# Performance work log

Hardware: AMD Instinct MI355X
Metric: run time of the kernel (lower is better)

The kernel has to match this reference:

```python
import jax, jax.numpy as jnp
import numpy as np

B, S, H, F, E, N, K = 2, 4096, 1024, 3584, 8, 2, 2


def setup_inputs() -> dict:
    key = jax.random.key(0)
    ks = jax.random.split(key, 6)
    scale_h = 1.0 / np.sqrt(H)
    scale_f = 1.0 / np.sqrt(F)
    return {
        "hidden_states": jax.random.normal(ks[0], (B, S, H), dtype=jnp.float32),
        "gate_w": jax.random.normal(ks[1], (E, H), dtype=jnp.float32) * scale_h,
        "gate2_w": jax.random.normal(ks[2], (N, H), dtype=jnp.float32) * scale_h,
        "w1": jax.random.normal(ks[3], (E, F, H), dtype=jnp.float32) * scale_h,
        "w2": jax.random.normal(ks[4], (E, H, F), dtype=jnp.float32) * scale_f,
        "w3": jax.random.normal(ks[5], (E, F, H), dtype=jnp.float32) * scale_h,
    }


def reference(hidden_states, gate_w, gate2_w, w1, w2, w3):
    b, s, h = hidden_states.shape
    x = hidden_states.reshape(-1, h)  # [T, H]

    # Router: real gate + null-expert gate, concatenated
    router_logits = jnp.concatenate([x @ gate_w.T, x @ gate2_w.T], axis=1)  # [T, E+N]
    rw = jax.nn.softmax(router_logits.astype(jnp.float32), axis=1)
    top_w, sel = jax.lax.top_k(rw, K)  # [T, K]

    # Null experts (idx >= E) get their raw weight; real experts are renormalized
    mask = sel < E
    sw = top_w * mask
    denom = sw.sum(axis=-1, keepdims=True)
    denom = jnp.where(denom == 0, 1.0, denom)
    weights = (sw / denom + top_w * (~mask)).astype(x.dtype)  # [T, K]

    # Per-(token, real-expert) combine weight; null experts drop out (one_hot -> 0)
    combine = jnp.einsum("tke,tk->et", jax.nn.one_hot(sel, E, dtype=x.dtype), weights)  # [E, T]

    def body(acc, p):
        w1e, w2e, w3e, cw = p
        hgate = jax.nn.silu(x @ w1e.T) * (x @ w3e.T)  # [T, F]
        return acc + cw[:, None] * (hgate @ w2e.T), None

    out, _ = jax.lax.scan(body, jnp.zeros_like(x), (w1, w2, w3, combine))
    return out.reshape(b, s, h), router_logits
```

## Files before the change

kernel.cpp:

```cpp
#include <hip/hip_runtime.h>
#include <hip/hip_bf16.h>

namespace {

constexpr int T_TOK = 8192;
constexpr int HDIM  = 1024;
constexpr int FDIM  = 3584;
constexpr int CAP_ROWS = 17408;
constexpr int MAXMT = CAP_ROWS / 128;

typedef __bf16 bf16x8 __attribute__((ext_vector_type(8)));
typedef float  f32x4  __attribute__((ext_vector_type(4)));

#define CFENCE() asm volatile("" ::: "memory")

__device__ inline unsigned short f2bf(float f) {
  union { float f; unsigned u; } a; a.f = f;
  unsigned r = a.u + 0x7fffu + ((a.u >> 16) & 1u);
  return (unsigned short)(r >> 16);
}

typedef const __attribute__((address_space(1))) void* gptr_t;
typedef __attribute__((address_space(3))) void* lptr_t;
__device__ inline void gload_lds16(const void* g, void* l) {
  __builtin_amdgcn_global_load_lds((gptr_t)g, (lptr_t)l, 16, 0, 0);
}

__global__ __launch_bounds__(256) void k_router(
    const float* __restrict__ x, const float* __restrict__ gw,
    const float* __restrict__ gw2, float* __restrict__ logits_out,
    int* __restrict__ sel, float* __restrict__ wts)
{
  int t = blockIdx.x * 4 + (threadIdx.x >> 6);
  int lane = threadIdx.x & 63;
  if (t >= T_TOK) return;
  const float* xr = x + (size_t)t * HDIM;
  float acc[10];
#pragma unroll
  for (int e = 0; e < 10; ++e) acc[e] = 0.f;
#pragma unroll
  for (int it = 0; it < 4; ++it) {
    int base = it * 256 + lane * 4;
    float4 xv = *reinterpret_cast<const float4*>(xr + base);
#pragma unroll
    for (int e = 0; e < 8; ++e) {
      float4 g = *reinterpret_cast<const float4*>(gw + e * HDIM + base);
      acc[e] += xv.x * g.x + xv.y * g.y + xv.z * g.z + xv.w * g.w;
    }
#pragma unroll
    for (int e = 0; e < 2; ++e) {
      float4 g = *reinterpret_cast<const float4*>(gw2 + e * HDIM + base);
      acc[8 + e] += xv.x * g.x + xv.y * g.y + xv.z * g.z + xv.w * g.w;
    }
  }
#pragma unroll
  for (int e = 0; e < 10; ++e) {
#pragma unroll
    for (int off = 32; off > 0; off >>= 1)
      acc[e] += __shfl_xor(acc[e], off, 64);
  }
  if (lane == 0) {
    float* lo = logits_out + (size_t)t * 10;
#pragma unroll
    for (int e = 0; e < 10; ++e) lo[e] = acc[e];
    float mx = acc[0];
#pragma unroll
    for (int e = 1; e < 10; ++e) mx = fmaxf(mx, acc[e]);
    float p[10], s = 0.f;
#pragma unroll
    for (int e = 0; e < 10; ++e) { p[e] = __expf(acc[e] - mx); s += p[e]; }
    float inv = 1.f / s;
#pragma unroll
    for (int e = 0; e < 10; ++e) p[e] *= inv;
    int i0 = 0;
    for (int e = 1; e < 10; ++e) if (p[e] > p[i0]) i0 = e;
    int i1 = (i0 == 0) ? 1 : 0;
    for (int e = 0; e < 10; ++e) if (e != i0 && p[e] > p[i1]) i1 = e;
    float w0 = p[i0], w1 = p[i1];
    bool r0 = i0 < 8, r1 = i1 < 8;
    float den = (r0 ? w0 : 0.f) + (r1 ? w1 : 0.f);
    if (den == 0.f) den = 1.f;
    sel[t * 2]     = i0; wts[t * 2]     = r0 ? w0 / den : 0.f;
    sel[t * 2 + 1] = i1; wts[t * 2 + 1] = r1 ? w1 / den : 0.f;
  }
}

__global__ __launch_bounds__(256) void k_histseg(
    const int* __restrict__ sel, int* __restrict__ meta)
{
  __shared__ int part[256][8];
  __shared__ int s_tile0[9];
  int tid = threadIdx.x;
  int c[8];
#pragma unroll
  for (int e = 0; e < 8; ++e) c[e] = 0;
  for (int i = 0; i < 64; ++i) {
    int v = sel[i * 256 + tid];
#pragma unroll
    for (int e = 0; e < 8; ++e) c[e] += (v == e);
  }
#pragma unroll
  for (int e = 0; e < 8; ++e) part[tid][e] = c[e];
  __syncthreads();
  for (int s = 128; s >= 1; s >>= 1) {
    if (tid < s) {
#pragma unroll
      for (int e = 0; e < 8; ++e) part[tid][e] += part[tid + s][e];
    }
    __syncthreads();
  }
  if (tid == 0) {
    int off = 0;
    for (int e = 0; e < 8; ++e) {
      int cnt = part[0][e];
      meta[e] = cnt;
      meta[8 + e] = 0;
      meta[16 + e] = off;
      s_tile0[e] = off >> 7;
      off += (cnt + 127) & ~127;
    }
    meta[24] = off;
    meta[25] = off >> 7;
    s_tile0[8] = off >> 7;
  }
  __syncthreads();
  int nt = s_tile0[8];
  if (tid < nt) {
    int e = 0;
    while (s_tile0[e + 1] <= tid) ++e;
    meta[32 + tid] = e;
  }
}

__global__ __launch_bounds__(256) void k_zeropad(
    const int* __restrict__ meta, unsigned short* __restrict__ xg)
{
  int e = blockIdx.x >> 7, r = blockIdx.x & 127;
  int c = meta[e];
  int pad = (c + 127) & ~127;
  if (c + r >= pad) return;
  size_t row = (size_t)meta[16 + e] + c + r;
  reinterpret_cast<ushort4*>(xg + row * HDIM)[threadIdx.x] = ushort4{0, 0, 0, 0};
}

__global__ __launch_bounds__(256) void k_scatter(
    const float* __restrict__ x, const int* __restrict__ sel,
    int* __restrict__ meta, int* __restrict__ pair_row,
    unsigned short* __restrict__ xg)
{
  __shared__ int s_cnt[8];
  __shared__ int s_base[8];
  __shared__ int s_row[256];
  int tid = threadIdx.x;
  int pair0 = blockIdx.x * 256;
  if (tid < 8) s_cnt[tid] = 0;
  __syncthreads();
  int e = sel[pair0 + tid];
  int rank = -1;
  if (e < 8) rank = atomicAdd(&s_cnt[e], 1);
  __syncthreads();
  if (tid < 8) {
    int c = s_cnt[tid];
    s_base[tid] = c > 0 ? atomicAdd(&meta[8 + tid], c) : 0;
  }
  __syncthreads();
  int row = (e < 8) ? meta[16 + e] + s_base[e] + rank : -1;
  pair_row[pair0 + tid] = row;
  s_row[tid] = row;
  __syncthreads();
  int wid = tid >> 6, lane = tid & 63;
  for (int i = wid; i < 256; i += 4) {
    int r = s_row[i];
    if (r < 0) continue;
    const float* xr = x + (size_t)((pair0 + i) >> 1) * HDIM;
    unsigned short* dst = xg + (size_t)r * HDIM;
#pragma unroll
    for (int it = 0; it < 4; ++it) {
      int base = it * 256 + lane * 4;
      float4 v = *reinterpret_cast<const float4*>(xr + base);
      ushort4 o{f2bf(v.x), f2bf(v.y), f2bf(v.z), f2bf(v.w)};
      *reinterpret_cast<ushort4*>(dst + base) = o;
    }
  }
}

__global__ __launch_bounds__(256) void k_conv3(
    const float* __restrict__ s1, const float* __restrict__ s3,
    const float* __restrict__ s2,
    unsigned short* __restrict__ d1, unsigned short* __restrict__ d3,
    unsigned short* __restrict__ d2,
    long long total, long long rl13, long long ss13,
    long long rl2, long long ss2)
{
  long long i = ((long long)blockIdx.x * 256 + threadIdx.x) * 8;
  if (i >= total) return;
  const float* src; unsigned short* dst; long long rowlen, sstride;
  if (blockIdx.y == 0)      { src = s1; dst = d1; rowlen = rl13; sstride = ss13; }
  else if (blockIdx.y == 1) { src = s3; dst = d3; rowlen = rl13; sstride = ss13; }
  else                      { src = s2; dst = d2; rowlen = rl2;  sstride = ss2;  }
  const float* sp;
  if (rowlen == sstride) {
    sp = src + i;
  } else {
    long long r = i / rowlen, c = i - r * rowlen;
    sp = src + r * sstride + c;
  }
  float4 a = reinterpret_cast<const float4*>(sp)[0];
  float4 b = reinterpret_cast<const float4*>(sp)[1];
  ushort4* d = reinterpret_cast<ushort4*>(dst + i);
  d[0] = ushort4{f2bf(a.x), f2bf(a.y), f2bf(a.z), f2bf(a.w)};
  d[1] = ushort4{f2bf(b.x), f2bf(b.y), f2bf(b.z), f2bf(b.w)};
}

__global__ __launch_bounds__(256) void k_gemm1(
    const unsigned short* __restrict__ xg,
    const unsigned short* __restrict__ wc1,
    const unsigned short* __restrict__ wc3,
    unsigned short* __restrict__ hg,
    const int* __restrict__ meta, int Fc)
{
  __shared__ __attribute__((aligned(128))) char lds[65536];

  int mt = blockIdx.y;
  if (mt >= meta[25]) return;
  int e = meta[32 + mt];
  int mrow0 = mt * 128;
  int fl0 = blockIdx.x * 64;

  int tid = threadIdx.x, wid = tid >> 6, lane = tid & 63;
  int lr = lane & 15, lg = lane >> 4;
  int wm = wid >> 1, wn = wid & 1;

  f32x4 acc1[4][2], acc3[4][2];
  const f32x4 zero = {0.f, 0.f, 0.f, 0.f};
#pragma unroll
  for (int m = 0; m < 4; ++m)
#pragma unroll
    for (int n = 0; n < 2; ++n) { acc1[m][n] = zero; acc3[m][n] = zero; }

  const unsigned short* w1p = wc1 + ((size_t)e * Fc + fl0) * HDIM;
  const unsigned short* w3p = wc3 + ((size_t)e * Fc + fl0) * HDIM;

  int srow = tid >> 3;
  int c8 = (tid & 7) ^ (srow & 7);

  const unsigned short* pa[4];
  const unsigned short* pb1[2];
  const unsigned short* pb3[2];
#pragma unroll
  for (int i = 0; i < 4; ++i)
    pa[i] = xg + (size_t)(mrow0 + i * 32 + srow) * HDIM + c8 * 8;
#pragma unroll
  for (int i = 0; i < 2; ++i) {
    pb1[i] = w1p + (size_t)(i * 32 + srow) * HDIM + c8 * 8;
    pb3[i] = w3p + (size_t)(i * 32 + srow) * HDIM + c8 * 8;
  }

  auto STAGE = [&](int buf) {
    char* base = lds + buf * 32768;
#pragma unroll
    for (int i = 0; i < 4; ++i) {
      gload_lds16(pa[i], base + i * 4096 + wid * 1024);
      pa[i] += 64;
    }
#pragma unroll
    for (int i = 0; i < 2; ++i) {
      gload_lds16(pb1[i], base + 16384 + i * 4096 + wid * 1024);
      pb1[i] += 64;
      gload_lds16(pb3[i], base + 24576 + i * 4096 + wid * 1024);
      pb3[i] += 64;
    }
  };

  auto COMPUTE = [&](int buf) {
    const char* base = lds + buf * 32768;
#pragma unroll
    for (int kk = 0; kk < 2; ++kk) {
      bf16x8 a[4], b1[2], b3[2];
#pragma unroll
      for (int m = 0; m < 4; ++m) {
        int r = wm * 64 + m * 16 + lr;
        int off = r * 128 + ((kk * 64 + lg * 16) ^ ((r & 7) << 4));
        a[m] = *reinterpret_cast<const bf16x8*>(base + off);
      }
#pragma unroll
      for (int n = 0; n < 2; ++n) {
        int r = wn * 32 + n * 16 + lr;
        int off = r * 128 + ((kk * 64 + lg * 16) ^ ((r & 7) << 4));
        b1[n] = *reinterpret_cast<const bf16x8*>(base + 16384 + off);
        b3[n] = *reinterpret_cast<const bf16x8*>(base + 24576 + off);
      }
#pragma unroll
      for (int m = 0; m < 4; ++m)
#pragma unroll
        for (int n = 0; n < 2; ++n) {
          acc1[m][n] = __builtin_amdgcn_mfma_f32_16x16x32_bf16(a[m], b1[n], acc1[m][n], 0, 0, 0);
          acc3[m][n] = __builtin_amdgcn_mfma_f32_16x16x32_bf16(a[m], b3[n], acc3[m][n], 0, 0, 0);
        }
    }
  };

  constexpr int NT = HDIM / 64;
  int cur = 0;
  STAGE(0);
#pragma unroll 1
  for (int t = 0; t < NT - 1; ++t) {
    STAGE(cur ^ 1);
    asm volatile("s_waitcnt vmcnt(8)" ::: "memory");
    __builtin_amdgcn_s_barrier();
    CFENCE();
    COMPUTE(cur);
    CFENCE();
    __builtin_amdgcn_s_barrier();
    cur ^= 1;
  }
  asm volatile("s_waitcnt vmcnt(0)" ::: "memory");
  __builtin_amdgcn_s_barrier();
  CFENCE();
  COMPUTE(cur);

#pragma unroll
  for (int m = 0; m < 4; ++m)
#pragma unroll
    for (int n = 0; n < 2; ++n) {
      int gcol = fl0 + wn * 32 + n * 16 + lr;
#pragma unroll
      for (int j = 0; j < 4; ++j) {
        int grow = mrow0 + wm * 64 + m * 16 + lg * 4 + j;
        float s1 = acc1[m][n][j];
        float s3 = acc3[m][n][j];
        float h = s1 / (1.f + __expf(-s1)) * s3;
        hg[(size_t)grow * Fc + gcol] = f2bf(h);
      }
    }
}

__global__ __launch_bounds__(256) void k_gemm2(
    const unsigned short* __restrict__ hg,
    const unsigned short* __restrict__ wc2,
    float* __restrict__ yrows, const int* __restrict__ meta,
    int Fc, int first)
{
  __shared__ __attribute__((aligned(128))) char lds[65536];

  int mt = blockIdx.y;
  if (mt >= meta[25]) return;
  int e = meta[32 + mt];
  int mrow0 = mt * 128;
  int hcol0 = blockIdx.x * 128;

  int tid = threadIdx.x, wid = tid >> 6, lane = tid & 63;
  int lr = lane & 15, lg = lane >> 4;
  int wm = wid >> 1, wn = wid & 1;

  f32x4 acc[4][4];
  const f32x4 zero = {0.f, 0.f, 0.f, 0.f};
#pragma unroll
  for (int m = 0; m < 4; ++m)
#pragma unroll
    for (int n = 0; n < 4; ++n) acc[m][n] = zero;

  const unsigned short* w2p = wc2 + ((size_t)e * HDIM + hcol0) * Fc;

  int srow = tid >> 3;
  int c8 = (tid & 7) ^ (srow & 7);

  const unsigned short* pa[4];
  const unsigned short* pb[4];
#pragma unroll
  for (int i = 0; i < 4; ++i) {
    pa[i] = hg + (size_t)(mrow0 + i * 32 + srow) * Fc + c8 * 8;
    pb[i] = w2p + (size_t)(i * 32 + srow) * Fc + c8 * 8;
  }

  auto STAGE = [&](int buf) {
    char* base = lds + buf * 32768;
#pragma unroll
    for (int i = 0; i < 4; ++i) {
      gload_lds16(pa[i], base + i * 4096 + wid * 1024);
      pa[i] += 64;
      gload_lds16(pb[i], base + 16384 + i * 4096 + wid * 1024);
      pb[i] += 64;
    }
  };

  auto COMPUTE = [&](int buf) {
    const char* base = lds + buf * 32768;
#pragma unroll
    for (int kk = 0; kk < 2; ++kk) {
      bf16x8 a[4], b[4];
#pragma unroll
      for (int m = 0; m < 4; ++m) {
        int r = wm * 64 + m * 16 + lr;
        int off = r * 128 + ((kk * 64 + lg * 16) ^ ((r & 7) << 4));
        a[m] = *reinterpret_cast<const bf16x8*>(base + off);
      }
#pragma unroll
      for (int n = 0; n < 4; ++n) {
        int r = wn * 64 + n * 16 + lr;
        int off = r * 128 + ((kk * 64 + lg * 16) ^ ((r & 7) << 4));
        b[n] = *reinterpret_cast<const bf16x8*>(base + 16384 + off);
      }
#pragma unroll
      for (int m = 0; m < 4; ++m)
#pragma unroll
        for (int n = 0; n < 4; ++n)
          acc[m][n] = __builtin_amdgcn_mfma_f32_16x16x32_bf16(a[m], b[n], acc[m][n], 0, 0, 0);
    }
  };

  int NT = Fc / 64;
  int cur = 0;
  STAGE(0);
#pragma unroll 1
  for (int t = 0; t < NT - 1; ++t) {
    STAGE(cur ^ 1);
    asm volatile("s_waitcnt vmcnt(8)" ::: "memory");
    __builtin_amdgcn_s_barrier();
    CFENCE();
    COMPUTE(cur);
    CFENCE();
    __builtin_amdgcn_s_barrier();
    cur ^= 1;
  }
  asm volatile("s_waitcnt vmcnt(0)" ::: "memory");
  __builtin_amdgcn_s_barrier();
  CFENCE();
  COMPUTE(cur);

#pragma unroll
  for (int m = 0; m < 4; ++m)
#pragma unroll
    for (int n = 0; n < 4; ++n) {
      int gcol = hcol0 + wn * 64 + n * 16 + lr;
#pragma unroll
      for (int j = 0; j < 4; ++j) {
        int grow = mrow0 + wm * 64 + m * 16 + lg * 4 + j;
        float* yp = yrows + (size_t)grow * HDIM + gcol;
        float v = acc[m][n][j];
        if (first) *yp = v; else *yp += v;
      }
    }
}

__global__ __launch_bounds__(256) void k_combine(
    const float* __restrict__ yrows, const int* __restrict__ pair_row,
    const float* __restrict__ wts, float* __restrict__ out)
{
  int t = blockIdx.x * 4 + (threadIdx.x >> 6);
  int lane = threadIdx.x & 63;
  if (t >= T_TOK) return;
  int r0 = pair_row[t * 2], r1 = pair_row[t * 2 + 1];
  float w0 = (r0 >= 0) ? wts[t * 2] : 0.f;
  float w1 = (r1 >= 0) ? wts[t * 2 + 1] : 0.f;
  const float* y0 = yrows + (size_t)(r0 >= 0 ? r0 : 0) * HDIM;
  const float* y1 = yrows + (size_t)(r1 >= 0 ? r1 : 0) * HDIM;
  float* op = out + (size_t)t * HDIM;
#pragma unroll
  for (int it = 0; it < 4; ++it) {
    int base = it * 256 + lane * 4;
    float4 a = *reinterpret_cast<const float4*>(y0 + base);
    float4 b = *reinterpret_cast<const float4*>(y1 + base);
    float4 r{w0 * a.x + w1 * b.x, w0 * a.y + w1 * b.y,
             w0 * a.z + w1 * b.z, w0 * a.w + w1 * b.w};
    *reinterpret_cast<float4*>(op + base) = r;
  }
}

}

extern "C" void kernel_launch(void* const* d_in, const int* in_sizes, int n_in,
                              void* d_out, int out_size, void* d_ws, size_t ws_size,
                              hipStream_t stream)
{
  const float* x   = (const float*)d_in[0];
  const float* gw  = (const float*)d_in[1];
  const float* gw2 = (const float*)d_in[2];
  const float* w1  = (const float*)d_in[3];
  const float* w2  = (const float*)d_in[4];
  const float* w3  = (const float*)d_in[5];
  float* out = (float*)d_out;
  float* logits_out = out + (size_t)T_TOK * HDIM;

  char* p = (char*)d_ws;
  int* meta = (int*)p;            p += 1024;
  int* sel = (int*)p;             p += T_TOK * 2 * sizeof(int);
  float* wts = (float*)p;         p += T_TOK * 2 * sizeof(float);
  int* pair_row = (int*)p;        p += T_TOK * 2 * sizeof(int);
  unsigned short* xg = (unsigned short*)p;  p += (size_t)CAP_ROWS * HDIM * 2;
  float* yrows = (float*)p;                 p += (size_t)CAP_ROWS * HDIM * 4;
  size_t fixed = (size_t)(p - (char*)d_ws);

  int nf = 28;
  const int opts[6] = {1, 2, 4, 7, 14, 28};
  for (int i = 0; i < 6; ++i) {
    size_t Fc_i = FDIM / opts[i];
    size_t need = fixed + 3 * 16384 * Fc_i + (size_t)CAP_ROWS * Fc_i * 2;
    if (need <= ws_size) { nf = opts[i]; break; }
  }
  int Fc = FDIM / nf;

  unsigned short* wc1 = (unsigned short*)p;  p += (size_t)16384 * Fc;
  unsigned short* wc3 = (unsigned short*)p;  p += (size_t)16384 * Fc;
  unsigned short* wc2 = (unsigned short*)p;  p += (size_t)16384 * Fc;
  unsigned short* hg  = (unsigned short*)p;

  k_router<<<T_TOK / 4, 256, 0, stream>>>(x, gw, gw2, logits_out, sel, wts);
  k_histseg<<<1, 256, 0, stream>>>(sel, meta);
  k_zeropad<<<1024, 256, 0, stream>>>(meta, xg);
  k_scatter<<<T_TOK * 2 / 256, 256, 0, stream>>>(x, sel, meta, pair_row, xg);

  long long total = 8LL * Fc * HDIM;
  int ncb = (int)(total / 8 / 256);
  for (int c = 0; c < nf; ++c) {
    long long c0 = (long long)c * Fc;
    k_conv3<<<dim3(ncb, 3), 256, 0, stream>>>(
        w1 + c0 * HDIM, w3 + c0 * HDIM, w2 + c0, wc1, wc3, wc2,
        total, (long long)Fc * HDIM, (long long)FDIM * HDIM,
        (long long)Fc, (long long)FDIM);

    k_gemm1<<<dim3(Fc / 64, MAXMT), 256, 0, stream>>>(xg, wc1, wc3, hg, meta, Fc);
    k_gemm2<<<dim3(HDIM / 128, MAXMT), 256, 0, stream>>>(hg, wc2, yrows, meta, Fc, c == 0 ? 1 : 0);
  }
  k_combine<<<T_TOK / 4, 256, 0, stream>>>(yrows, pair_row, wts, out);
}
```

Before: 529.2 us.

## Enlarge expert GEMM tiles to 256 rows with 8-wave phased MFMA pipeline

Both grouped GEMMs move from 128-row tiles with 4 waves to 256-row tiles with 8 waves (512 threads). Expert segments are now padded to 256 rows, and the A and B staging is split so loads interleave with four barrier-separated MFMA phases, using raised wave priority during the MFMA bursts. The larger tiles reuse each loaded weight tile across more rows and give more MFMA work per LDS load. The costs are more padding rows per expert, much larger LDS use (up to 128 KB), which limits occupancy, and Fc must now divide by 128 in gemm1.

Result: slower. 548.9 us (+3.7%).

```diff
diff --git a/kernel.cpp b/kernel.cpp
--- a/kernel.cpp
+++ b/kernel.cpp
@@ -6,13 +6,11 @@
 constexpr int T_TOK = 8192;
 constexpr int HDIM  = 1024;
 constexpr int FDIM  = 3584;
-constexpr int CAP_ROWS = 17408;
-constexpr int MAXMT = CAP_ROWS / 128;
+constexpr int CAP_ROWS = 18432;
+constexpr int MAXMT = CAP_ROWS / 256;
 
 typedef __bf16 bf16x8 __attribute__((ext_vector_type(8)));
 typedef float  f32x4  __attribute__((ext_vector_type(4)));
-
-#define CFENCE() asm volatile("" ::: "memory")
 
 __device__ inline unsigned short f2bf(float f) {
   union { float f; unsigned u; } a; a.f = f;
@@ -25,6 +23,8 @@
 __device__ inline void gload_lds16(const void* g, void* l) {
   __builtin_amdgcn_global_load_lds((gptr_t)g, (lptr_t)l, 16, 0, 0);
 }
+
+#define MFMA16(a, b, c) __builtin_amdgcn_mfma_f32_16x16x32_bf16(a, b, c, 0, 0, 0)
 
 __global__ __launch_bounds__(256) void k_router(
     const float* __restrict__ x, const float* __restrict__ gw,
@@ -116,12 +116,12 @@
       meta[e] = cnt;
       meta[8 + e] = 0;
       meta[16 + e] = off;
-      s_tile0[e] = off >> 7;
-      off += (cnt + 127) & ~127;
+      s_tile0[e] = off >> 8;
+      off += (cnt + 255) & ~255;
     }
     meta[24] = off;
-    meta[25] = off >> 7;
-    s_tile0[8] = off >> 7;
+    meta[25] = off >> 8;
+    s_tile0[8] = off >> 8;
   }
   __syncthreads();
   int nt = s_tile0[8];
@@ -135,9 +135,9 @@
 __global__ __launch_bounds__(256) void k_zeropad(
     const int* __restrict__ meta, unsigned short* __restrict__ xg)
 {
-  int e = blockIdx.x >> 7, r = blockIdx.x & 127;
+  int e = blockIdx.x >> 8, r = blockIdx.x & 255;
   int c = meta[e];
-  int pad = (c + 127) & ~127;
+  int pad = (c + 255) & ~255;
   if (c + r >= pad) return;
   size_t row = (size_t)meta[16 + e] + c + r;
   reinterpret_cast<ushort4*>(xg + row * HDIM)[threadIdx.x] = ushort4{0, 0, 0, 0};
@@ -212,121 +212,138 @@
   d[1] = ushort4{f2bf(b.x), f2bf(b.y), f2bf(b.z), f2bf(b.w)};
 }
 
-__global__ __launch_bounds__(256) void k_gemm1(
+__global__ __launch_bounds__(512, 2) void k_gemm1(
     const unsigned short* __restrict__ xg,
     const unsigned short* __restrict__ wc1,
     const unsigned short* __restrict__ wc3,
     unsigned short* __restrict__ hg,
     const int* __restrict__ meta, int Fc)
 {
-  __shared__ __attribute__((aligned(128))) char lds[65536];
+  __shared__ __attribute__((aligned(128))) char lds[131072];
 
   int mt = blockIdx.y;
   if (mt >= meta[25]) return;
   int e = meta[32 + mt];
-  int mrow0 = mt * 128;
-  int fl0 = blockIdx.x * 64;
-
-  int tid = threadIdx.x, wid = tid >> 6, lane = tid & 63;
+  int mrow0 = mt * 256;
+  int fl0 = blockIdx.x * 128;
+
+  int tid = threadIdx.x, lane = tid & 63, wid = tid >> 6;
   int lr = lane & 15, lg = lane >> 4;
-  int wm = wid >> 1, wn = wid & 1;
-
-  f32x4 acc1[4][2], acc3[4][2];
+  int wr = wid >> 2, wc = wid & 3;
+
+  f32x4 acc1[8][2], acc3[8][2];
   const f32x4 zero = {0.f, 0.f, 0.f, 0.f};
 #pragma unroll
-  for (int m = 0; m < 4; ++m)
+  for (int m = 0; m < 8; ++m)
 #pragma unroll
     for (int n = 0; n < 2; ++n) { acc1[m][n] = zero; acc3[m][n] = zero; }
 
-  const unsigned short* w1p = wc1 + ((size_t)e * Fc + fl0) * HDIM;
-  const unsigned short* w3p = wc3 + ((size_t)e * Fc + fl0) * HDIM;
-
-  int srow = tid >> 3;
-  int c8 = (tid & 7) ^ (srow & 7);
+  int r0 = tid >> 3;
+  int csw = ((tid & 7) ^ (r0 & 7)) * 8;
+  int dst0 = tid * 16;
 
   const unsigned short* pa[4];
   const unsigned short* pb1[2];
   const unsigned short* pb3[2];
-#pragma unroll
-  for (int i = 0; i < 4; ++i)
-    pa[i] = xg + (size_t)(mrow0 + i * 32 + srow) * HDIM + c8 * 8;
-#pragma unroll
-  for (int i = 0; i < 2; ++i) {
-    pb1[i] = w1p + (size_t)(i * 32 + srow) * HDIM + c8 * 8;
-    pb3[i] = w3p + (size_t)(i * 32 + srow) * HDIM + c8 * 8;
-  }
-
-  auto STAGE = [&](int buf) {
-    char* base = lds + buf * 32768;
+  {
+    const unsigned short* Ab  = xg + (size_t)mrow0 * HDIM;
+    const unsigned short* B1b = wc1 + ((size_t)e * Fc + fl0) * HDIM;
+    const unsigned short* B3b = wc3 + ((size_t)e * Fc + fl0) * HDIM;
+#pragma unroll
+    for (int h = 0; h < 2; ++h)
+#pragma unroll
+      for (int q = 0; q < 2; ++q)
+        pa[h * 2 + q] = Ab + (size_t)(h * 128 + q * 64 + r0) * HDIM + csw;
+#pragma unroll
+    for (int q = 0; q < 2; ++q) {
+      pb1[q] = B1b + (size_t)(q * 64 + r0) * HDIM + csw;
+      pb3[q] = B3b + (size_t)(q * 64 + r0) * HDIM + csw;
+    }
+  }
+
+  auto STAGE_A = [&](int buf) {
+    char* b = lds + buf * 65536;
 #pragma unroll
     for (int i = 0; i < 4; ++i) {
-      gload_lds16(pa[i], base + i * 4096 + wid * 1024);
+      gload_lds16(pa[i], b + (i >> 1) * 16384 + (i & 1) * 8192 + dst0);
       pa[i] += 64;
     }
-#pragma unroll
-    for (int i = 0; i < 2; ++i) {
-      gload_lds16(pb1[i], base + 16384 + i * 4096 + wid * 1024);
-      pb1[i] += 64;
-      gload_lds16(pb3[i], base + 24576 + i * 4096 + wid * 1024);
-      pb3[i] += 64;
-    }
   };
-
-  auto COMPUTE = [&](int buf) {
-    const char* base = lds + buf * 32768;
-#pragma unroll
-    for (int kk = 0; kk < 2; ++kk) {
-      bf16x8 a[4], b1[2], b3[2];
-#pragma unroll
-      for (int m = 0; m < 4; ++m) {
-        int r = wm * 64 + m * 16 + lr;
-        int off = r * 128 + ((kk * 64 + lg * 16) ^ ((r & 7) << 4));
-        a[m] = *reinterpret_cast<const bf16x8*>(base + off);
+  auto STAGE_B = [&](int buf) {
+    char* b = lds + buf * 65536;
+#pragma unroll
+    for (int q = 0; q < 2; ++q) {
+      gload_lds16(pb1[q], b + 32768 + q * 8192 + dst0);
+      pb1[q] += 64;
+      gload_lds16(pb3[q], b + 49152 + q * 8192 + dst0);
+      pb3[q] += 64;
+    }
+  };
+
+  const int fxor = (lr & 7) << 4;
+  bf16x8 b1f[2], b3f[2];
+
+  auto PHASE = [&](int buf, int kk, int mh, bool ldB) {
+    const char* bb = lds + buf * 65536;
+    const char* ab = bb + wr * 16384;
+    int kbyte = (kk * 64 + lg * 16) ^ fxor;
+    bf16x8 af[4];
+#pragma unroll
+    for (int i = 0; i < 4; ++i) {
+      int ra = (mh * 4 + i) * 16 + lr;
+      af[i] = *reinterpret_cast<const bf16x8*>(ab + ra * 128 + kbyte);
+    }
+    if (ldB) {
+#pragma unroll
+      for (int n = 0; n < 2; ++n) {
+        int off = (wc * 32 + n * 16 + lr) * 128 + kbyte;
+        b1f[n] = *reinterpret_cast<const bf16x8*>(bb + 32768 + off);
+        b3f[n] = *reinterpret_cast<const bf16x8*>(bb + 49152 + off);
       }
+    }
+    __builtin_amdgcn_s_barrier();
+    asm volatile("s_waitcnt lgkmcnt(0)" ::: "memory");
+    __builtin_amdgcn_sched_barrier(0);
+    __builtin_amdgcn_s_setprio(1);
+#pragma unroll
+    for (int i = 0; i < 4; ++i)
 #pragma unroll
       for (int n = 0; n < 2; ++n) {
-        int r = wn * 32 + n * 16 + lr;
-        int off = r * 128 + ((kk * 64 + lg * 16) ^ ((r & 7) << 4));
-        b1[n] = *reinterpret_cast<const bf16x8*>(base + 16384 + off);
-        b3[n] = *reinterpret_cast<const bf16x8*>(base + 24576 + off);
+        acc1[mh * 4 + i][n] = MFMA16(af[i], b1f[n], acc1[mh * 4 + i][n]);
+        acc3[mh * 4 + i][n] = MFMA16(af[i], b3f[n], acc3[mh * 4 + i][n]);
       }
-#pragma unroll
-      for (int m = 0; m < 4; ++m)
-#pragma unroll
-        for (int n = 0; n < 2; ++n) {
-          acc1[m][n] = __builtin_amdgcn_mfma_f32_16x16x32_bf16(a[m], b1[n], acc1[m][n], 0, 0, 0);
-          acc3[m][n] = __builtin_amdgcn_mfma_f32_16x16x32_bf16(a[m], b3[n], acc3[m][n], 0, 0, 0);
-        }
-    }
+    __builtin_amdgcn_s_setprio(0);
   };
 
   constexpr int NT = HDIM / 64;
-  int cur = 0;
-  STAGE(0);
-#pragma unroll 1
-  for (int t = 0; t < NT - 1; ++t) {
-    STAGE(cur ^ 1);
-    asm volatile("s_waitcnt vmcnt(8)" ::: "memory");
-    __builtin_amdgcn_s_barrier();
-    CFENCE();
-    COMPUTE(cur);
-    CFENCE();
-    __builtin_amdgcn_s_barrier();
-    cur ^= 1;
-  }
+  STAGE_A(0); STAGE_B(0);
   asm volatile("s_waitcnt vmcnt(0)" ::: "memory");
   __builtin_amdgcn_s_barrier();
-  CFENCE();
-  COMPUTE(cur);
-
-#pragma unroll
-  for (int m = 0; m < 4; ++m)
+#pragma unroll 1
+  for (int t = 0; t < NT; ++t) {
+    int c = t & 1;
+    bool st = (t < NT - 1);
+    if (st) STAGE_A(c ^ 1);
+    PHASE(c, 0, 0, true);
+    __builtin_amdgcn_s_barrier();
+    if (st) STAGE_B(c ^ 1);
+    PHASE(c, 0, 1, false);
+    __builtin_amdgcn_s_barrier();
+    PHASE(c, 1, 0, true);
+    __builtin_amdgcn_s_barrier();
+    PHASE(c, 1, 1, false);
+    asm volatile("s_waitcnt vmcnt(0)" ::: "memory");
+    __builtin_amdgcn_s_barrier();
+  }
+
+#pragma unroll
+  for (int m = 0; m < 8; ++m)
 #pragma unroll
     for (int n = 0; n < 2; ++n) {
-      int gcol = fl0 + wn * 32 + n * 16 + lr;
+      int gcol = fl0 + wc * 32 + n * 16 + lr;
 #pragma unroll
       for (int j = 0; j < 4; ++j) {
-        int grow = mrow0 + wm * 64 + m * 16 + lg * 4 + j;
+        int grow = mrow0 + wr * 128 + m * 16 + lg * 4 + j;
         float s1 = acc1[m][n][j];
         float s3 = acc3[m][n][j];
         float h = s1 / (1.f + __expf(-s1)) * s3;
@@ -335,107 +352,128 @@
     }
 }
 
-__global__ __launch_bounds__(256) void k_gemm2(
+__global__ __launch_bounds__(512, 2) void k_gemm2(
     const unsigned short* __restrict__ hg,
     const unsigned short* __restrict__ wc2,
     float* __restrict__ yrows, const int* __restrict__ meta,
     int Fc, int first)
 {
-  __shared__ __attribute__((aligned(128))) char lds[65536];
+  __shared__ __attribute__((aligned(128))) char lds[98304];
 
   int mt = blockIdx.y;
   if (mt >= meta[25]) return;
   int e = meta[32 + mt];
-  int mrow0 = mt * 128;
+  int mrow0 = mt * 256;
   int hcol0 = blockIdx.x * 128;
 
-  int tid = threadIdx.x, wid = tid >> 6, lane = tid & 63;
+  int tid = threadIdx.x, lane = tid & 63, wid = tid >> 6;
   int lr = lane & 15, lg = lane >> 4;
-  int wm = wid >> 1, wn = wid & 1;
-
-  f32x4 acc[4][4];
+  int wr = wid >> 2, wc = wid & 3;
+
+  f32x4 acc[8][2];
   const f32x4 zero = {0.f, 0.f, 0.f, 0.f};
 #pragma unroll
-  for (int m = 0; m < 4; ++m)
-#pragma unroll
-    for (int n = 0; n < 4; ++n) acc[m][n] = zero;
-
-  const unsigned short* w2p = wc2 + ((size_t)e * HDIM + hcol0) * Fc;
-
-  int srow = tid >> 3;
-  int c8 = (tid & 7) ^ (srow & 7);
+  for (int m = 0; m < 8; ++m)
+#pragma unroll
+    for (int n = 0; n < 2; ++n) acc[m][n] = zero;
+
+  int r0 = tid >> 3;
+  int csw = ((tid & 7) ^ (r0 & 7)) * 8;
+  int dst0 = tid * 16;
 
   const unsigned short* pa[4];
-  const unsigned short* pb[4];
-#pragma unroll
-  for (int i = 0; i < 4; ++i) {
-    pa[i] = hg + (size_t)(mrow0 + i * 32 + srow) * Fc + c8 * 8;
-    pb[i] = w2p + (size_t)(i * 32 + srow) * Fc + c8 * 8;
-  }
-
-  auto STAGE = [&](int buf) {
-    char* base = lds + buf * 32768;
+  const unsigned short* pb[2];
+  {
+    const unsigned short* Ab = hg + (size_t)mrow0 * Fc;
+    const unsigned short* Bb = wc2 + ((size_t)e * HDIM + hcol0) * Fc;
+#pragma unroll
+    for (int h = 0; h < 2; ++h)
+#pragma unroll
+      for (int q = 0; q < 2; ++q)
+        pa[h * 2 + q] = Ab + (size_t)(h * 128 + q * 64 + r0) * Fc + csw;
+#pragma unroll
+    for (int q = 0; q < 2; ++q)
+      pb[q] = Bb + (size_t)(q * 64 + r0) * Fc + csw;
+  }
+
+  auto STAGE_A = [&](int buf) {
+    char* b = lds + buf * 49152;
 #pragma unroll
     for (int i = 0; i < 4; ++i) {
-      gload_lds16(pa[i], base + i * 4096 + wid * 1024);
+      gload_lds16(pa[i], b + (i >> 1) * 16384 + (i & 1) * 8192 + dst0);
       pa[i] += 64;
-      gload_lds16(pb[i], base + 16384 + i * 4096 + wid * 1024);
-      pb[i] += 64;
     }
   };
-
-  auto COMPUTE = [&](int buf) {
-    const char* base = lds + buf * 32768;
-#pragma unroll
-    for (int kk = 0; kk < 2; ++kk) {
-      bf16x8 a[4], b[4];
-#pragma unroll
-      for (int m = 0; m < 4; ++m) {
-        int r = wm * 64 + m * 16 + lr;
-        int off = r * 128 + ((kk * 64 + lg * 16) ^ ((r & 7) << 4));
-        a[m] = *reinterpret_cast<const bf16x8*>(base + off);
+  auto STAGE_B = [&](int buf) {
+    char* b = lds + buf * 49152;
+#pragma unroll
+    for (int q = 0; q < 2; ++q) {
+      gload_lds16(pb[q], b + 32768 + q * 8192 + dst0);
+      pb[q] += 64;
+    }
+  };
+
+  const int fxor = (lr & 7) << 4;
+  bf16x8 bf[2];
+
+  auto PHASE = [&](int buf, int kk, int mh, bool ldB) {
+    const char* bb = lds + buf * 49152;
+    const char* ab = bb + wr * 16384;
+    int kbyte = (kk * 64 + lg * 16) ^ fxor;
+    bf16x8 af[4];
+#pragma unroll
+    for (int i = 0; i < 4; ++i) {
+      int ra = (mh * 4 + i) * 16 + lr;
+      af[i] = *reinterpret_cast<const bf16x8*>(ab + ra * 128 + kbyte);
+    }
+    if (ldB) {
+#pragma unroll
+      for (int n = 0; n < 2; ++n) {
+        int off = (wc * 32 + n * 16 + lr) * 128 + kbyte;
+        bf[n] = *reinterpret_cast<const bf16x8*>(bb + 32768 + off);
       }
-#pragma unroll
-      for (int n = 0; n < 4; ++n) {
-        int r = wn * 64 + n * 16 + lr;
-        int off = r * 128 + ((kk * 64 + lg * 16) ^ ((r & 7) << 4));
-        b[n] = *reinterpret_cast<const bf16x8*>(base + 16384 + off);
-      }
-#pragma unroll
-      for (int m = 0; m < 4; ++m)
-#pragma unroll
-        for (int n = 0; n < 4; ++n)
-          acc[m][n] = __builtin_amdgcn_mfma_f32_16x16x32_bf16(a[m], b[n], acc[m][n], 0, 0, 0);
-    }
+    }
+    __builtin_amdgcn_s_barrier();
+    asm volatile("s_waitcnt lgkmcnt(0)" ::: "memory");
+    __builtin_amdgcn_sched_barrier(0);
+    __builtin_amdgcn_s_setprio(1);
+#pragma unroll
+    for (int i = 0; i < 4; ++i)
+#pragma unroll
+      for (int n = 0; n < 2; ++n)
+        acc[mh * 4 + i][n] = MFMA16(af[i], bf[n], acc[mh * 4 + i][n]);
+    __builtin_amdgcn_s_setprio(0);
   };
 
   int NT = Fc / 64;
-  int cur = 0;
-  STAGE(0);
-#pragma unroll 1
-  for (int t = 0; t < NT - 1; ++t) {
-    STAGE(cur ^ 1);
-    asm volatile("s_waitcnt vmcnt(8)" ::: "memory");
-    __builtin_amdgcn_s_barrier();
-    CFENCE();
-    COMPUTE(cur);
-    CFENCE();
-    __builtin_amdgcn_s_barrier();
-    cur ^= 1;
-  }
+  STAGE_A(0); STAGE_B(0);
   asm volatile("s_waitcnt vmcnt(0)" ::: "memory");
   __builtin_amdgcn_s_barrier();
-  CFENCE();
-  COMPUTE(cur);
-
-#pragma unroll
-  for (int m = 0; m < 4; ++m)
-#pragma unroll
-    for (int n = 0; n < 4; ++n) {
-      int gcol = hcol0 + wn * 64 + n * 16 + lr;
+#pragma unroll 1
+  for (int t = 0; t < NT; ++t) {
+    int c = t & 1;
+    bool st = (t < NT - 1);
+    if (st) STAGE_A(c ^ 1);
+    PHASE(c, 0, 0, true);
+    __builtin_amdgcn_s_barrier();
+    if (st) STAGE_B(c ^ 1);
+    PHASE(c, 0, 1, false);
+    __builtin_amdgcn_s_barrier();
+    PHASE(c, 1, 0, true);
+    __builtin_amdgcn_s_barrier();
+    PHASE(c, 1, 1, false);
+    asm volatile("s_waitcnt vmcnt(0)" ::: "memory");
+    __builtin_amdgcn_s_barrier();
+  }
+
+#pragma unroll
+  for (int m = 0; m < 8; ++m)
+#pragma unroll
+    for (int n = 0; n < 2; ++n) {
+      int gcol = hcol0 + wc * 32 + n * 16 + lr;
 #pragma unroll
       for (int j = 0; j < 4; ++j) {
-        int grow = mrow0 + wm * 64 + m * 16 + lg * 4 + j;
+        int grow = mrow0 + wr * 128 + m * 16 + lg * 4 + j;
         float* yp = yrows + (size_t)grow * HDIM + gcol;
         float v = acc[m][n][j];
         if (first) *yp = v; else *yp += v;
@@ -507,7 +545,7 @@
 
   k_router<<<T_TOK / 4, 256, 0, stream>>>(x, gw, gw2, logits_out, sel, wts);
   k_histseg<<<1, 256, 0, stream>>>(sel, meta);
-  k_zeropad<<<1024, 256, 0, stream>>>(meta, xg);
+  k_zeropad<<<2048, 256, 0, stream>>>(meta, xg);
   k_scatter<<<T_TOK * 2 / 256, 256, 0, stream>>>(x, sel, meta, pair_row, xg);
 
   long long total = 8LL * Fc * HDIM;
@@ -519,8 +557,8 @@
         total, (long long)Fc * HDIM, (long long)FDIM * HDIM,
         (long long)Fc, (long long)FDIM);
 
-    k_gemm1<<<dim3(Fc / 64, MAXMT), 256, 0, stream>>>(xg, wc1, wc3, hg, meta, Fc);
-    k_gemm2<<<dim3(HDIM / 128, MAXMT), 256, 0, stream>>>(hg, wc2, yrows, meta, Fc, c == 0 ? 1 : 0);
+    k_gemm1<<<dim3(Fc / 128, MAXMT), 512, 0, stream>>>(xg, wc1, wc3, hg, meta, Fc);
+    k_gemm2<<<dim3(HDIM / 128, MAXMT), 512, 0, stream>>>(hg, wc2, yrows, meta, Fc, c == 0 ? 1 : 0);
   }
   k_combine<<<T_TOK / 4, 256, 0, stream>>>(yrows, pair_row, wts, out);
 }
```

## Gather token rows in gemm1 via index table and store expert outputs in bf16

Applied to the files above, without the earlier changes.

Replaces the materialized per-expert scatter of bf16 token rows with a dense bf16 copy of x plus a row-to-token index, so gemm1 gathers A rows directly during its loads. Padding rows point at token 0 instead of being zero-filled. The per-row expert output buffer changes from fp32 to bf16, which halves its traffic in gemm2 and combine but rounds the partial sums at every F-chunk. gemm1 also drops its double-buffered LDS pipeline for a simple single-buffer loop with a barrier per step, which exposes load latency.

Result: slower. 573.4 us (+8.4%).

```diff
diff --git a/kernel.cpp b/kernel.cpp
--- a/kernel.cpp
+++ b/kernel.cpp
@@ -18,6 +18,9 @@
   union { float f; unsigned u; } a; a.f = f;
   unsigned r = a.u + 0x7fffu + ((a.u >> 16) & 1u);
   return (unsigned short)(r >> 16);
+}
+__device__ inline float bf2f(unsigned short u) {
+  union { unsigned u; float f; } a; a.u = (unsigned)u << 16; return a.f;
 }
 
 typedef const __attribute__((address_space(1))) void* gptr_t;
@@ -86,10 +89,13 @@
 }
 
 __global__ __launch_bounds__(256) void k_histseg(
-    const int* __restrict__ sel, int* __restrict__ meta)
+    const int* __restrict__ sel, int* __restrict__ meta,
+    int* __restrict__ rowtok)
 {
   __shared__ int part[256][8];
   __shared__ int s_tile0[9];
+  __shared__ int s_off[8];
+  __shared__ int s_c[8];
   int tid = threadIdx.x;
   int c[8];
 #pragma unroll
@@ -116,6 +122,8 @@
       meta[e] = cnt;
       meta[8 + e] = 0;
       meta[16 + e] = off;
+      s_off[e] = off;
+      s_c[e] = cnt;
       s_tile0[e] = off >> 7;
       off += (cnt + 127) & ~127;
     }
@@ -130,27 +138,21 @@
     while (s_tile0[e + 1] <= tid) ++e;
     meta[32 + tid] = e;
   }
-}
-
-__global__ __launch_bounds__(256) void k_zeropad(
-    const int* __restrict__ meta, unsigned short* __restrict__ xg)
-{
-  int e = blockIdx.x >> 7, r = blockIdx.x & 127;
-  int c = meta[e];
-  int pad = (c + 127) & ~127;
-  if (c + r >= pad) return;
-  size_t row = (size_t)meta[16 + e] + c + r;
-  reinterpret_cast<ushort4*>(xg + row * HDIM)[threadIdx.x] = ushort4{0, 0, 0, 0};
-}
-
-__global__ __launch_bounds__(256) void k_scatter(
-    const float* __restrict__ x, const int* __restrict__ sel,
-    int* __restrict__ meta, int* __restrict__ pair_row,
-    unsigned short* __restrict__ xg)
+  for (int idx = tid; idx < 8 * 128; idx += 256) {
+    int e = idx >> 7, j = idx & 127;
+    int cnt = s_c[e];
+    int pad = (cnt + 127) & ~127;
+    int pos = cnt + j;
+    if (pos < pad) rowtok[s_off[e] + pos] = 0;
+  }
+}
+
+__global__ __launch_bounds__(256) void k_rank(
+    const int* __restrict__ sel, int* __restrict__ meta,
+    int* __restrict__ pair_row, int* __restrict__ rowtok)
 {
   __shared__ int s_cnt[8];
   __shared__ int s_base[8];
-  __shared__ int s_row[256];
   int tid = threadIdx.x;
   int pair0 = blockIdx.x * 256;
   if (tid < 8) s_cnt[tid] = 0;
@@ -166,22 +168,18 @@
   __syncthreads();
   int row = (e < 8) ? meta[16 + e] + s_base[e] + rank : -1;
   pair_row[pair0 + tid] = row;
-  s_row[tid] = row;
-  __syncthreads();
-  int wid = tid >> 6, lane = tid & 63;
-  for (int i = wid; i < 256; i += 4) {
-    int r = s_row[i];
-    if (r < 0) continue;
-    const float* xr = x + (size_t)((pair0 + i) >> 1) * HDIM;
-    unsigned short* dst = xg + (size_t)r * HDIM;
-#pragma unroll
-    for (int it = 0; it < 4; ++it) {
-      int base = it * 256 + lane * 4;
-      float4 v = *reinterpret_cast<const float4*>(xr + base);
-      ushort4 o{f2bf(v.x), f2bf(v.y), f2bf(v.z), f2bf(v.w)};
-      *reinterpret_cast<ushort4*>(dst + base) = o;
-    }
-  }
+  if (row >= 0) rowtok[row] = (pair0 + tid) >> 1;
+}
+
+__global__ __launch_bounds__(256) void k_convx(
+    const float* __restrict__ x, unsigned short* __restrict__ xgd)
+{
+  long long i = ((long long)blockIdx.x * 256 + threadIdx.x) * 8;
+  float4 a = reinterpret_cast<const float4*>(x + i)[0];
+  float4 b = reinterpret_cast<const float4*>(x + i)[1];
+  ushort4* d = reinterpret_cast<ushort4*>(xgd + i);
+  d[0] = ushort4{f2bf(a.x), f2bf(a.y), f2bf(a.z), f2bf(a.w)};
+  d[1] = ushort4{f2bf(b.x), f2bf(b.y), f2bf(b.z), f2bf(b.w)};
 }
 
 __global__ __launch_bounds__(256) void k_conv3(
@@ -213,13 +211,16 @@
 }
 
 __global__ __launch_bounds__(256) void k_gemm1(
-    const unsigned short* __restrict__ xg,
+    const unsigned short* __restrict__ xgd,
+    const int* __restrict__ rowtok,
     const unsigned short* __restrict__ wc1,
     const unsigned short* __restrict__ wc3,
     unsigned short* __restrict__ hg,
     const int* __restrict__ meta, int Fc)
 {
-  __shared__ __attribute__((aligned(128))) char lds[65536];
+  __shared__ unsigned short As[128 * 64];
+  __shared__ unsigned short B1s[64 * 64];
+  __shared__ unsigned short B3s[64 * 64];
 
   int mt = blockIdx.y;
   if (mt >= meta[25]) return;
@@ -245,35 +246,25 @@
   int c8 = (tid & 7) ^ (srow & 7);
 
   const unsigned short* pa[4];
-  const unsigned short* pb1[2];
-  const unsigned short* pb3[2];
-#pragma unroll
-  for (int i = 0; i < 4; ++i)
-    pa[i] = xg + (size_t)(mrow0 + i * 32 + srow) * HDIM + c8 * 8;
-#pragma unroll
-  for (int i = 0; i < 2; ++i) {
-    pb1[i] = w1p + (size_t)(i * 32 + srow) * HDIM + c8 * 8;
-    pb3[i] = w3p + (size_t)(i * 32 + srow) * HDIM + c8 * 8;
-  }
-
-  auto STAGE = [&](int buf) {
-    char* base = lds + buf * 32768;
-#pragma unroll
-    for (int i = 0; i < 4; ++i) {
-      gload_lds16(pa[i], base + i * 4096 + wid * 1024);
-      pa[i] += 64;
-    }
+#pragma unroll
+  for (int i = 0; i < 4; ++i) {
+    int tok = rowtok[mrow0 + i * 32 + srow];
+    pa[i] = xgd + (size_t)tok * HDIM + c8 * 8;
+  }
+
+  for (int k0 = 0; k0 < HDIM; k0 += 64) {
+#pragma unroll
+    for (int i = 0; i < 4; ++i)
+      gload_lds16(pa[i] + k0, (char*)As + i * 4096 + wid * 1024);
 #pragma unroll
     for (int i = 0; i < 2; ++i) {
-      gload_lds16(pb1[i], base + 16384 + i * 4096 + wid * 1024);
-      pb1[i] += 64;
-      gload_lds16(pb3[i], base + 24576 + i * 4096 + wid * 1024);
-      pb3[i] += 64;
-    }
-  };
-
-  auto COMPUTE = [&](int buf) {
-    const char* base = lds + buf * 32768;
+      gload_lds16(w1p + (size_t)(i * 32 + srow) * HDIM + k0 + c8 * 8,
+                  (char*)B1s + i * 4096 + wid * 1024);
+      gload_lds16(w3p + (size_t)(i * 32 + srow) * HDIM + k0 + c8 * 8,
+                  (char*)B3s + i * 4096 + wid * 1024);
+    }
+    __syncthreads();
+
 #pragma unroll
     for (int kk = 0; kk < 2; ++kk) {
       bf16x8 a[4], b1[2], b3[2];
@@ -281,14 +272,14 @@
       for (int m = 0; m < 4; ++m) {
         int r = wm * 64 + m * 16 + lr;
         int off = r * 128 + ((kk * 64 + lg * 16) ^ ((r & 7) << 4));
-        a[m] = *reinterpret_cast<const bf16x8*>(base + off);
+        a[m] = *reinterpret_cast<const bf16x8*>((const char*)As + off);
       }
 #pragma unroll
       for (int n = 0; n < 2; ++n) {
         int r = wn * 32 + n * 16 + lr;
         int off = r * 128 + ((kk * 64 + lg * 16) ^ ((r & 7) << 4));
-        b1[n] = *reinterpret_cast<const bf16x8*>(base + 16384 + off);
-        b3[n] = *reinterpret_cast<const bf16x8*>(base + 24576 + off);
+        b1[n] = *reinterpret_cast<const bf16x8*>((const char*)B1s + off);
+        b3[n] = *reinterpret_cast<const bf16x8*>((const char*)B3s + off);
       }
 #pragma unroll
       for (int m = 0; m < 4; ++m)
@@ -298,26 +289,8 @@
           acc3[m][n] = __builtin_amdgcn_mfma_f32_16x16x32_bf16(a[m], b3[n], acc3[m][n], 0, 0, 0);
         }
     }
-  };
-
-  constexpr int NT = HDIM / 64;
-  int cur = 0;
-  STAGE(0);
-#pragma unroll 1
-  for (int t = 0; t < NT - 1; ++t) {
-    STAGE(cur ^ 1);
-    asm volatile("s_waitcnt vmcnt(8)" ::: "memory");
-    __builtin_amdgcn_s_barrier();
-    CFENCE();
-    COMPUTE(cur);
-    CFENCE();
-    __builtin_amdgcn_s_barrier();
-    cur ^= 1;
-  }
-  asm volatile("s_waitcnt vmcnt(0)" ::: "memory");
-  __builtin_amdgcn_s_barrier();
-  CFENCE();
-  COMPUTE(cur);
+    __syncthreads();
+  }
 
 #pragma unroll
   for (int m = 0; m < 4; ++m)
@@ -338,7 +311,7 @@
 __global__ __launch_bounds__(256) void k_gemm2(
     const unsigned short* __restrict__ hg,
     const unsigned short* __restrict__ wc2,
-    float* __restrict__ yrows, const int* __restrict__ meta,
+    unsigned short* __restrict__ yrows, const int* __restrict__ meta,
     int Fc, int first)
 {
   __shared__ __attribute__((aligned(128))) char lds[65536];
@@ -436,15 +409,16 @@
 #pragma unroll
       for (int j = 0; j < 4; ++j) {
         int grow = mrow0 + wm * 64 + m * 16 + lg * 4 + j;
-        float* yp = yrows + (size_t)grow * HDIM + gcol;
+        unsigned short* yp = yrows + (size_t)grow * HDIM + gcol;
         float v = acc[m][n][j];
-        if (first) *yp = v; else *yp += v;
+        if (!first) v += bf2f(*yp);
+        *yp = f2bf(v);
       }
     }
 }
 
 __global__ __launch_bounds__(256) void k_combine(
-    const float* __restrict__ yrows, const int* __restrict__ pair_row,
+    const unsigned short* __restrict__ yrows, const int* __restrict__ pair_row,
     const float* __restrict__ wts, float* __restrict__ out)
 {
   int t = blockIdx.x * 4 + (threadIdx.x >> 6);
@@ -453,17 +427,26 @@
   int r0 = pair_row[t * 2], r1 = pair_row[t * 2 + 1];
   float w0 = (r0 >= 0) ? wts[t * 2] : 0.f;
   float w1 = (r1 >= 0) ? wts[t * 2 + 1] : 0.f;
-  const float* y0 = yrows + (size_t)(r0 >= 0 ? r0 : 0) * HDIM;
-  const float* y1 = yrows + (size_t)(r1 >= 0 ? r1 : 0) * HDIM;
+  const unsigned short* y0 = yrows + (size_t)(r0 >= 0 ? r0 : 0) * HDIM;
+  const unsigned short* y1 = yrows + (size_t)(r1 >= 0 ? r1 : 0) * HDIM;
   float* op = out + (size_t)t * HDIM;
 #pragma unroll
-  for (int it = 0; it < 4; ++it) {
-    int base = it * 256 + lane * 4;
-    float4 a = *reinterpret_cast<const float4*>(y0 + base);
-    float4 b = *reinterpret_cast<const float4*>(y1 + base);
-    float4 r{w0 * a.x + w1 * b.x, w0 * a.y + w1 * b.y,
-             w0 * a.z + w1 * b.z, w0 * a.w + w1 * b.w};
-    *reinterpret_cast<float4*>(op + base) = r;
+  for (int it = 0; it < 2; ++it) {
+    int base = it * 512 + lane * 8;
+    ushort4 a0 = *reinterpret_cast<const ushort4*>(y0 + base);
+    ushort4 a1 = *reinterpret_cast<const ushort4*>(y0 + base + 4);
+    ushort4 b0 = *reinterpret_cast<const ushort4*>(y1 + base);
+    ushort4 b1 = *reinterpret_cast<const ushort4*>(y1 + base + 4);
+    float4 r0v{w0 * bf2f(a0.x) + w1 * bf2f(b0.x),
+               w0 * bf2f(a0.y) + w1 * bf2f(b0.y),
+               w0 * bf2f(a0.z) + w1 * bf2f(b0.z),
+               w0 * bf2f(a0.w) + w1 * bf2f(b0.w)};
+    float4 r1v{w0 * bf2f(a1.x) + w1 * bf2f(b1.x),
+               w0 * bf2f(a1.y) + w1 * bf2f(b1.y),
+               w0 * bf2f(a1.z) + w1 * bf2f(b1.z),
+               w0 * bf2f(a1.w) + w1 * bf2f(b1.w)};
+    *reinterpret_cast<float4*>(op + base) = r0v;
+    *reinterpret_cast<float4*>(op + base + 4) = r1v;
   }
 }
 
@@ -487,8 +470,9 @@
   int* sel = (int*)p;             p += T_TOK * 2 * sizeof(int);
   float* wts = (float*)p;         p += T_TOK * 2 * sizeof(float);
   int* pair_row = (int*)p;        p += T_TOK * 2 * sizeof(int);
-  unsigned short* xg = (unsigned short*)p;  p += (size_t)CAP_ROWS * HDIM * 2;
-  float* yrows = (float*)p;                 p += (size_t)CAP_ROWS * HDIM * 4;
+  int* rowtok = (int*)p;          p += CAP_ROWS * sizeof(int);
+  unsigned short* xgd = (unsigned short*)p;   p += (size_t)T_TOK * HDIM * 2;
+  unsigned short* yrows = (unsigned short*)p; p += (size_t)CAP_ROWS * HDIM * 2;
   size_t fixed = (size_t)(p - (char*)d_ws);
 
   int nf = 28;
@@ -506,9 +490,9 @@
   unsigned short* hg  = (unsigned short*)p;
 
   k_router<<<T_TOK / 4, 256, 0, stream>>>(x, gw, gw2, logits_out, sel, wts);
-  k_histseg<<<1, 256, 0, stream>>>(sel, meta);
-  k_zeropad<<<1024, 256, 0, stream>>>(meta, xg);
-  k_scatter<<<T_TOK * 2 / 256, 256, 0, stream>>>(x, sel, meta, pair_row, xg);
+  k_histseg<<<1, 256, 0, stream>>>(sel, meta, rowtok);
+  k_rank<<<T_TOK * 2 / 256, 256, 0, stream>>>(sel, meta, pair_row, rowtok);
+  k_convx<<<T_TOK * HDIM / 8 / 256, 256, 0, stream>>>(x, xgd);
 
   long long total = 8LL * Fc * HDIM;
   int ncb = (int)(total / 8 / 256);
@@ -519,7 +503,7 @@
         total, (long long)Fc * HDIM, (long long)FDIM * HDIM,
         (long long)Fc, (long long)FDIM);
 
-    k_gemm1<<<dim3(Fc / 64, MAXMT), 256, 0, stream>>>(xg, wc1, wc3, hg, meta, Fc);
+    k_gemm1<<<dim3(Fc / 64, MAXMT), 256, 0, stream>>>(xgd, rowtok, wc1, wc3, hg, meta, Fc);
     k_gemm2<<<dim3(HDIM / 128, MAXMT), 256, 0, stream>>>(hg, wc2, yrows, meta, Fc, c == 0 ? 1 : 0);
   }
   k_combine<<<T_TOK / 4, 256, 0, stream>>>(yrows, pair_row, wts, out);
```
